# Kernel tuning notes

Hardware: AMD Instinct MI355X
Metric: run time of the kernel (lower is better)

Reference implementation:

```python
import jax, jax.numpy as jnp
import numpy as np

B = 2          # batch size (fixed constant; torch code derives it from coords[:,0].max()+1)
C = 64         # NUM_BEV_FEATURES
NX = NY = 480  # grid_size, nz == 1
NXC = NYC = 960  # hardcoded 'cen' grid


def _make_coords(key, P, b, ny, nx):
    kb, ky, kx = jax.random.split(key, 3)
    bi = jax.random.randint(kb, (P,), 0, b, dtype=jnp.int32)
    z = jnp.zeros((P,), jnp.int32)
    y = jax.random.randint(ky, (P,), 0, ny, dtype=jnp.int32)
    x = jax.random.randint(kx, (P,), 0, nx, dtype=jnp.int32)
    return jnp.stack([bi, z, y, x], axis=1)


def setup_inputs() -> dict:
    key = jax.random.key(0)
    ks = jax.random.split(key, 8)
    return {
        "radar_cen_pillar_features": jax.random.normal(ks[0], (8000, C), jnp.float32),
        "radar_cen_coords": _make_coords(ks[1], 8000, B, NYC, NXC),
        "lidar_cen_pillar_features": jax.random.normal(ks[2], (30000, C), jnp.float32),
        "lidar_cen_coords": _make_coords(ks[3], 30000, B, NYC, NXC),
        "lidar_pillar_features": jax.random.normal(ks[4], (30000, C), jnp.float32),
        "lidar_coords": _make_coords(ks[5], 30000, B, NY, NX),
        "radar_pillar_features": jax.random.normal(ks[6], (8000, C), jnp.float32),
        "radar_coords": _make_coords(ks[7], 8000, B, NY, NX),
    }


def _scatter_bev(feat, coords, ny, nx):
    # feat [P, C], coords [P, 4] = (b, z, y, x); flat index = z + y*nx + x (nz==1 so z==0)
    idx = coords[:, 1] + coords[:, 2] * nx + coords[:, 3]
    grid = jnp.zeros((B, ny * nx, feat.shape[1]), feat.dtype)
    grid = grid.at[coords[:, 0], idx].set(feat)
    # -> [B, C, ny, nx]
    return grid.transpose(0, 2, 1).reshape(B, feat.shape[1], ny, nx)


def _maxpool2(x):
    # AdaptiveMaxPool2d(480) on 960x960 == 2x2 max pool
    b, c, h, w = x.shape
    return x.reshape(b, c, h // 2, 2, w // 2, 2).max(axis=(3, 5))


def reference(radar_cen_pillar_features, radar_cen_coords,
              lidar_cen_pillar_features, lidar_cen_coords,
              lidar_pillar_features, lidar_coords,
              radar_pillar_features, radar_coords):
    radar_cen = _maxpool2(_scatter_bev(radar_cen_pillar_features, radar_cen_coords, NYC, NXC))
    lidar_cen = _maxpool2(_scatter_bev(lidar_cen_pillar_features, lidar_cen_coords, NYC, NXC))
    lidar = _scatter_bev(lidar_pillar_features, lidar_coords, NY, NX)
    radar = _scatter_bev(radar_pillar_features, radar_coords, NY, NX)
    cat = jnp.concatenate(
        [jnp.concatenate([lidar, lidar_cen], axis=1),
         jnp.concatenate([radar, radar_cen], axis=1)], axis=1)
    return lidar, radar, cat
```

## Files before the change

### kernel.cpp

```cpp
#include <hip/hip_runtime.h>

#define NX   480
#define NXC  960
#define NS   (480*480)
#define NSC  (960*960)
#define CC   64
#define BB   2

typedef float f4v __attribute__((ext_vector_type(4)));

__device__ __forceinline__ void nt_store4(float* p, float a, float b, float c, float d) {
    f4v v = {a, b, c, d};
    __builtin_nontemporal_store(v, (f4v*)p);
}

__device__ __forceinline__ f4v ld4(int w, const float* __restrict__ f, int c) {
    f4v z = {0.0f, 0.0f, 0.0f, 0.0f};
    if (w < 0) return z;
    return *(const f4v*)(f + (size_t)w * CC + c);
}

__device__ __forceinline__ f4v max4(f4v a, f4v b) {
    f4v r;
    r.x = fmaxf(a.x, b.x); r.y = fmaxf(a.y, b.y);
    r.z = fmaxf(a.z, b.z); r.w = fmaxf(a.w, b.w);
    return r;
}

struct SrcDesc { const int* coords; int* winner; int P; int nx; int ns; };

__global__ void __launch_bounds__(256)
scatter_winner4(SrcDesc s0, SrcDesc s1, SrcDesc s2, SrcDesc s3) {
    SrcDesc d = (blockIdx.y == 0) ? s0 : (blockIdx.y == 1) ? s1
              : (blockIdx.y == 2) ? s2 : s3;
    int p = blockIdx.x * 256 + threadIdx.x;
    if (p >= d.P) return;
    int b = d.coords[4*p + 0];
    int y = d.coords[4*p + 2];
    int x = d.coords[4*p + 3];
    atomicMax(&d.winner[b*d.ns + y*d.nx + x], p);
}

__global__ void __launch_bounds__(256)
dense_write(const float* __restrict__ lf,  const float* __restrict__ rf,
            const float* __restrict__ lcf, const float* __restrict__ rcf,
            const int* __restrict__ wl,  const int* __restrict__ wr,
            const int* __restrict__ wlc, const int* __restrict__ wrc,
            float* __restrict__ out_l, float* __restrict__ out_r,
            float* __restrict__ out_cat) {
    int s = (blockIdx.x * 256 + threadIdx.x) * 4;
    int b = blockIdx.y;
    int c0 = blockIdx.z * 16;

    int4 v_l = *(const int4*)(wl + (size_t)b*NS + s);
    int4 v_r = *(const int4*)(wr + (size_t)b*NS + s);
    int wla[4] = {v_l.x, v_l.y, v_l.z, v_l.w};
    int wra[4] = {v_r.x, v_r.y, v_r.z, v_r.w};

    int py = s / NX, px = s - py * NX;
    int y0 = py * 2, x0 = px * 2;
    const int* blc = wlc + (size_t)b * NSC;
    const int* brc = wrc + (size_t)b * NSC;
    int4 lt0 = *(const int4*)(blc + (size_t)y0*NXC + x0);
    int4 lt1 = *(const int4*)(blc + (size_t)y0*NXC + x0 + 4);
    int4 lb0 = *(const int4*)(blc + (size_t)(y0+1)*NXC + x0);
    int4 lb1 = *(const int4*)(blc + (size_t)(y0+1)*NXC + x0 + 4);
    int4 rt0 = *(const int4*)(brc + (size_t)y0*NXC + x0);
    int4 rt1 = *(const int4*)(brc + (size_t)y0*NXC + x0 + 4);
    int4 rb0 = *(const int4*)(brc + (size_t)(y0+1)*NXC + x0);
    int4 rb1 = *(const int4*)(brc + (size_t)(y0+1)*NXC + x0 + 4);
    int lct[8] = {lt0.x, lt0.y, lt0.z, lt0.w, lt1.x, lt1.y, lt1.z, lt1.w};
    int lcb[8] = {lb0.x, lb0.y, lb0.z, lb0.w, lb1.x, lb1.y, lb1.z, lb1.w};
    int rct[8] = {rt0.x, rt0.y, rt0.z, rt0.w, rt1.x, rt1.y, rt1.z, rt1.w};
    int rcb[8] = {rb0.x, rb0.y, rb0.z, rb0.w, rb1.x, rb1.y, rb1.z, rb1.w};

    size_t so  = (size_t)b * CC  * NS + s;
    size_t co  = (size_t)b * 256 * NS + s;

    #pragma unroll 1
    for (int g = 0; g < 4; ++g) {
        int c = c0 + g * 4;
        f4v vl[4], vr[4], vlc[4], vrc[4];
        #pragma unroll
        for (int j = 0; j < 4; ++j) {
            vl[j] = ld4(wla[j], lf, c);
            vr[j] = ld4(wra[j], rf, c);
            f4v a = ld4(lct[2*j], lcf, c);
            a = max4(a, ld4(lct[2*j+1], lcf, c));
            a = max4(a, ld4(lcb[2*j],   lcf, c));
            a = max4(a, ld4(lcb[2*j+1], lcf, c));
            vlc[j] = a;
            f4v m = ld4(rct[2*j], rcf, c);
            m = max4(m, ld4(rct[2*j+1], rcf, c));
            m = max4(m, ld4(rcb[2*j],   rcf, c));
            m = max4(m, ld4(rcb[2*j+1], rcf, c));
            vrc[j] = m;
        }
        #pragma unroll
        for (int k = 0; k < 4; ++k) {
            size_t cs = (size_t)(c + k) * NS;
            nt_store4(out_l   + so + cs,                      vl[0][k],  vl[1][k],  vl[2][k],  vl[3][k]);
            nt_store4(out_r   + so + cs,                      vr[0][k],  vr[1][k],  vr[2][k],  vr[3][k]);
            nt_store4(out_cat + co + cs,                      vl[0][k],  vl[1][k],  vl[2][k],  vl[3][k]);
            nt_store4(out_cat + co + (size_t)64*NS  + cs,     vlc[0][k], vlc[1][k], vlc[2][k], vlc[3][k]);
            nt_store4(out_cat + co + (size_t)128*NS + cs,     vr[0][k],  vr[1][k],  vr[2][k],  vr[3][k]);
            nt_store4(out_cat + co + (size_t)192*NS + cs,     vrc[0][k], vrc[1][k], vrc[2][k], vrc[3][k]);
        }
    }
}

extern "C" void kernel_launch(void* const* d_in, const int* in_sizes, int n_in,
                              void* d_out, int out_size, void* d_ws, size_t ws_size,
                              hipStream_t stream) {
    const float* rc_feat   = (const float*)d_in[0];
    const int*   rc_coords = (const int*)  d_in[1];
    const float* lc_feat   = (const float*)d_in[2];
    const int*   lc_coords = (const int*)  d_in[3];
    const float* l_feat    = (const float*)d_in[4];
    const int*   l_coords  = (const int*)  d_in[5];
    const float* r_feat    = (const float*)d_in[6];
    const int*   r_coords  = (const int*)  d_in[7];

    int P_rc = in_sizes[0] / CC;
    int P_lc = in_sizes[2] / CC;
    int P_l  = in_sizes[4] / CC;
    int P_r  = in_sizes[6] / CC;

    float* out_lidar = (float*)d_out;
    float* out_radar = out_lidar + (size_t)BB*CC*NS;
    float* out_cat   = out_radar + (size_t)BB*CC*NS;

    int* w_l  = (int*)d_ws;
    int* w_r  = w_l  + BB*NS;
    int* w_lc = w_r  + BB*NS;
    int* w_rc = w_lc + BB*NSC;
    size_t ws_bytes = (size_t)(2*BB*NS + 2*BB*NSC) * sizeof(int);

    hipMemsetAsync(d_ws, 0xFF, ws_bytes, stream);

    SrcDesc s_l  = { l_coords,  w_l,  P_l,  NX,  NS  };
    SrcDesc s_r  = { r_coords,  w_r,  P_r,  NX,  NS  };
    SrcDesc s_lc = { lc_coords, w_lc, P_lc, NXC, NSC };
    SrcDesc s_rc = { rc_coords, w_rc, P_rc, NXC, NSC };
    int maxP = max(max(P_l, P_r), max(P_lc, P_rc));
    dim3 wgrid((maxP + 255) / 256, 4);
    scatter_winner4<<<wgrid, 256, 0, stream>>>(s_l, s_r, s_lc, s_rc);

    dim3 grid(NS / (256 * 4), BB, 4);
    dense_write<<<grid, 256, 0, stream>>>(l_feat, r_feat, lc_feat, rc_feat,
                                          w_l, w_r, w_lc, w_rc,
                                          out_lidar, out_radar, out_cat);
}
```

Baseline: 730.6 us.

## Replace dense gather-write with memset plus sparse scatter of occupied cells

Instead of a dense pass that reads winner maps for every output cell and writes all channels, the output is zero-filled with hipMemsetAsync and a sparse kernel writes only the cells that hold a winning pillar. The scatter kernel also records a per-pooled-cell winner for the center grids, so each pooled cell is handled once. This drops the dense winner-map reads and the pillar-feature gathers in favour of a memset plus scattered 4-byte stores with a large channel stride. Those stores are poorly coalesced, and the output is still written in full by the memset.

```diff
diff --git a/kernel.cpp b/kernel.cpp
--- a/kernel.cpp
+++ b/kernel.cpp
@@ -9,17 +9,6 @@
 
 typedef float f4v __attribute__((ext_vector_type(4)));
 
-__device__ __forceinline__ void nt_store4(float* p, float a, float b, float c, float d) {
-    f4v v = {a, b, c, d};
-    __builtin_nontemporal_store(v, (f4v*)p);
-}
-
-__device__ __forceinline__ f4v ld4(int w, const float* __restrict__ f, int c) {
-    f4v z = {0.0f, 0.0f, 0.0f, 0.0f};
-    if (w < 0) return z;
-    return *(const f4v*)(f + (size_t)w * CC + c);
-}
-
 __device__ __forceinline__ f4v max4(f4v a, f4v b) {
     f4v r;
     r.x = fmaxf(a.x, b.x); r.y = fmaxf(a.y, b.y);
@@ -27,7 +16,7 @@
     return r;
 }
 
-struct SrcDesc { const int* coords; int* winner; int P; int nx; int ns; };
+struct SrcDesc { const int* coords; int* winner; int* pooled; int P; int nx; int ns; };
 
 __global__ void __launch_bounds__(256)
 scatter_winner4(SrcDesc s0, SrcDesc s1, SrcDesc s2, SrcDesc s3) {
@@ -39,73 +28,71 @@
     int y = d.coords[4*p + 2];
     int x = d.coords[4*p + 3];
     atomicMax(&d.winner[b*d.ns + y*d.nx + x], p);
+    if (d.pooled)
+        atomicMax(&d.pooled[b*NS + (y>>1)*NX + (x>>1)], p);
 }
 
 __global__ void __launch_bounds__(256)
-dense_write(const float* __restrict__ lf,  const float* __restrict__ rf,
-            const float* __restrict__ lcf, const float* __restrict__ rcf,
-            const int* __restrict__ wl,  const int* __restrict__ wr,
-            const int* __restrict__ wlc, const int* __restrict__ wrc,
-            float* __restrict__ out_l, float* __restrict__ out_r,
-            float* __restrict__ out_cat) {
-    int s = (blockIdx.x * 256 + threadIdx.x) * 4;
-    int b = blockIdx.y;
-    int c0 = blockIdx.z * 16;
+sparse_write(const float* __restrict__ lf,  const float* __restrict__ rf,
+             const float* __restrict__ lcf, const float* __restrict__ rcf,
+             const int* __restrict__ l_coords,  const int* __restrict__ r_coords,
+             const int* __restrict__ lc_coords, const int* __restrict__ rc_coords,
+             const int* __restrict__ wl,  const int* __restrict__ wr,
+             const int* __restrict__ wlc, const int* __restrict__ wrc,
+             const int* __restrict__ wplc, const int* __restrict__ wprc,
+             int P_l, int P_r, int P_lc, int P_rc,
+             float* __restrict__ out_l, float* __restrict__ out_r,
+             float* __restrict__ out_cat)
+{
+    int idx = blockIdx.x * 256 + threadIdx.x;
+    int p = idx >> 4;
+    int q = idx & 15;
+    int job = blockIdx.y;
 
-    int4 v_l = *(const int4*)(wl + (size_t)b*NS + s);
-    int4 v_r = *(const int4*)(wr + (size_t)b*NS + s);
-    int wla[4] = {v_l.x, v_l.y, v_l.z, v_l.w};
-    int wra[4] = {v_r.x, v_r.y, v_r.z, v_r.w};
-
-    int py = s / NX, px = s - py * NX;
-    int y0 = py * 2, x0 = px * 2;
-    const int* blc = wlc + (size_t)b * NSC;
-    const int* brc = wrc + (size_t)b * NSC;
-    int4 lt0 = *(const int4*)(blc + (size_t)y0*NXC + x0);
-    int4 lt1 = *(const int4*)(blc + (size_t)y0*NXC + x0 + 4);
-    int4 lb0 = *(const int4*)(blc + (size_t)(y0+1)*NXC + x0);
-    int4 lb1 = *(const int4*)(blc + (size_t)(y0+1)*NXC + x0 + 4);
-    int4 rt0 = *(const int4*)(brc + (size_t)y0*NXC + x0);
-    int4 rt1 = *(const int4*)(brc + (size_t)y0*NXC + x0 + 4);
-    int4 rb0 = *(const int4*)(brc + (size_t)(y0+1)*NXC + x0);
-    int4 rb1 = *(const int4*)(brc + (size_t)(y0+1)*NXC + x0 + 4);
-    int lct[8] = {lt0.x, lt0.y, lt0.z, lt0.w, lt1.x, lt1.y, lt1.z, lt1.w};
-    int lcb[8] = {lb0.x, lb0.y, lb0.z, lb0.w, lb1.x, lb1.y, lb1.z, lb1.w};
-    int rct[8] = {rt0.x, rt0.y, rt0.z, rt0.w, rt1.x, rt1.y, rt1.z, rt1.w};
-    int rcb[8] = {rb0.x, rb0.y, rb0.z, rb0.w, rb1.x, rb1.y, rb1.z, rb1.w};
-
-    size_t so  = (size_t)b * CC  * NS + s;
-    size_t co  = (size_t)b * 256 * NS + s;
-
-    #pragma unroll 1
-    for (int g = 0; g < 4; ++g) {
-        int c = c0 + g * 4;
-        f4v vl[4], vr[4], vlc[4], vrc[4];
-        #pragma unroll
-        for (int j = 0; j < 4; ++j) {
-            vl[j] = ld4(wla[j], lf, c);
-            vr[j] = ld4(wra[j], rf, c);
-            f4v a = ld4(lct[2*j], lcf, c);
-            a = max4(a, ld4(lct[2*j+1], lcf, c));
-            a = max4(a, ld4(lcb[2*j],   lcf, c));
-            a = max4(a, ld4(lcb[2*j+1], lcf, c));
-            vlc[j] = a;
-            f4v m = ld4(rct[2*j], rcf, c);
-            m = max4(m, ld4(rct[2*j+1], rcf, c));
-            m = max4(m, ld4(rcb[2*j],   rcf, c));
-            m = max4(m, ld4(rcb[2*j+1], rcf, c));
-            vrc[j] = m;
-        }
+    if (job < 2) {
+        const float* f      = job ? rf       : lf;
+        const int*   coords = job ? r_coords : l_coords;
+        const int*   w      = job ? wr       : wl;
+        int          P      = job ? P_r      : P_l;
+        if (p >= P) return;
+        int4 c = *(const int4*)(coords + 4*p);
+        int b  = c.x;
+        int sp = c.z * NX + c.w;
+        if (w[b*NS + sp] != p) return;
+        f4v v = *(const f4v*)(f + (size_t)p*CC + 4*q);
+        float* o1 = (job ? out_r : out_l)
+                  + (size_t)b*CC*NS  + (size_t)(4*q)*NS + sp;
+        float* o2 = out_cat
+                  + (size_t)b*256*NS + (size_t)((job ? 128 : 0) + 4*q)*NS + sp;
         #pragma unroll
         for (int k = 0; k < 4; ++k) {
-            size_t cs = (size_t)(c + k) * NS;
-            nt_store4(out_l   + so + cs,                      vl[0][k],  vl[1][k],  vl[2][k],  vl[3][k]);
-            nt_store4(out_r   + so + cs,                      vr[0][k],  vr[1][k],  vr[2][k],  vr[3][k]);
-            nt_store4(out_cat + co + cs,                      vl[0][k],  vl[1][k],  vl[2][k],  vl[3][k]);
-            nt_store4(out_cat + co + (size_t)64*NS  + cs,     vlc[0][k], vlc[1][k], vlc[2][k], vlc[3][k]);
-            nt_store4(out_cat + co + (size_t)128*NS + cs,     vr[0][k],  vr[1][k],  vr[2][k],  vr[3][k]);
-            nt_store4(out_cat + co + (size_t)192*NS + cs,     vrc[0][k], vrc[1][k], vrc[2][k], vrc[3][k]);
+            __builtin_nontemporal_store(v[k], o1 + (size_t)k*NS);
+            __builtin_nontemporal_store(v[k], o2 + (size_t)k*NS);
         }
+    } else {
+        const float* f      = (job == 3) ? rcf       : lcf;
+        const int*   coords = (job == 3) ? rc_coords : lc_coords;
+        const int*   w      = (job == 3) ? wrc       : wlc;
+        const int*   wp     = (job == 3) ? wprc      : wplc;
+        int          P      = (job == 3) ? P_rc      : P_lc;
+        if (p >= P) return;
+        int4 c = *(const int4*)(coords + 4*p);
+        int b  = c.x;
+        int oy = c.z >> 1, ox = c.w >> 1;
+        int o  = oy * NX + ox;
+        if (wp[b*NS + o] != p) return;
+        const int* wg = w + (size_t)b*NSC + (size_t)(oy*2)*NXC + ox*2;
+        int w00 = wg[0], w01 = wg[1], w10 = wg[NXC], w11 = wg[NXC + 1];
+        f4v a = {0.0f, 0.0f, 0.0f, 0.0f};
+        if (w00 >= 0) a = max4(a, *(const f4v*)(f + (size_t)w00*CC + 4*q));
+        if (w01 >= 0) a = max4(a, *(const f4v*)(f + (size_t)w01*CC + 4*q));
+        if (w10 >= 0) a = max4(a, *(const f4v*)(f + (size_t)w10*CC + 4*q));
+        if (w11 >= 0) a = max4(a, *(const f4v*)(f + (size_t)w11*CC + 4*q));
+        float* o2 = out_cat
+                  + (size_t)b*256*NS + (size_t)((job == 3 ? 192 : 64) + 4*q)*NS + o;
+        #pragma unroll
+        for (int k = 0; k < 4; ++k)
+            __builtin_nontemporal_store(a[k], o2 + (size_t)k*NS);
     }
 }
 
@@ -130,24 +117,32 @@
     float* out_radar = out_lidar + (size_t)BB*CC*NS;
     float* out_cat   = out_radar + (size_t)BB*CC*NS;
 
-    int* w_l  = (int*)d_ws;
-    int* w_r  = w_l  + BB*NS;
-    int* w_lc = w_r  + BB*NS;
-    int* w_rc = w_lc + BB*NSC;
-    size_t ws_bytes = (size_t)(2*BB*NS + 2*BB*NSC) * sizeof(int);
+    int* w_l   = (int*)d_ws;
+    int* w_r   = w_l   + (size_t)BB*NS;
+    int* w_plc = w_r   + (size_t)BB*NS;
+    int* w_prc = w_plc + (size_t)BB*NS;
+    int* w_lc  = w_prc + (size_t)BB*NS;
+    int* w_rc  = w_lc  + (size_t)BB*NSC;
+    size_t ws_bytes = ((size_t)4*BB*NS + (size_t)2*BB*NSC) * sizeof(int);
 
     hipMemsetAsync(d_ws, 0xFF, ws_bytes, stream);
 
-    SrcDesc s_l  = { l_coords,  w_l,  P_l,  NX,  NS  };
-    SrcDesc s_r  = { r_coords,  w_r,  P_r,  NX,  NS  };
-    SrcDesc s_lc = { lc_coords, w_lc, P_lc, NXC, NSC };
-    SrcDesc s_rc = { rc_coords, w_rc, P_rc, NXC, NSC };
+    size_t out_bytes = (size_t)BB * NS * (2*CC + 256) * sizeof(float);
+    hipMemsetAsync(d_out, 0, out_bytes, stream);
+
+    SrcDesc s_l  = { l_coords,  w_l,  nullptr, P_l,  NX,  NS  };
+    SrcDesc s_r  = { r_coords,  w_r,  nullptr, P_r,  NX,  NS  };
+    SrcDesc s_lc = { lc_coords, w_lc, w_plc,   P_lc, NXC, NSC };
+    SrcDesc s_rc = { rc_coords, w_rc, w_prc,   P_rc, NXC, NSC };
     int maxP = max(max(P_l, P_r), max(P_lc, P_rc));
     dim3 wgrid((maxP + 255) / 256, 4);
     scatter_winner4<<<wgrid, 256, 0, stream>>>(s_l, s_r, s_lc, s_rc);
 
-    dim3 grid(NS / (256 * 4), BB, 4);
-    dense_write<<<grid, 256, 0, stream>>>(l_feat, r_feat, lc_feat, rc_feat,
-                                          w_l, w_r, w_lc, w_rc,
-                                          out_lidar, out_radar, out_cat);
+    dim3 sgrid((maxP * 16 + 255) / 256, 4);
+    sparse_write<<<sgrid, 256, 0, stream>>>(
+        l_feat, r_feat, lc_feat, rc_feat,
+        l_coords, r_coords, lc_coords, rc_coords,
+        w_l, w_r, w_lc, w_rc, w_plc, w_prc,
+        P_l, P_r, P_lc, P_rc,
+        out_lidar, out_radar, out_cat);
 }
```

Result: slower. 1.017 ms (+39.2%).

## Split dense write into separate direct and pooled-center kernels per source

Applied to the files above, without the earlier changes.

Replaces the single dense kernel, which handled all four sources for a 16-channel slice, with two kernels. One copies the direct lidar/radar features to both outputs and the other max-pools the center grids into the concat tensor, each thread now covering all 64 channels of one source. The aim is lower register pressure and less divergent index loading per thread, and less redundant re-reading of winner indices across channel slices. The cost is an extra kernel launch and fewer blocks per launch, so there is less parallelism to hide memory latency.

```diff
diff --git a/kernel.cpp b/kernel.cpp
--- a/kernel.cpp
+++ b/kernel.cpp
@@ -42,69 +42,80 @@
 }
 
 __global__ void __launch_bounds__(256)
-dense_write(const float* __restrict__ lf,  const float* __restrict__ rf,
-            const float* __restrict__ lcf, const float* __restrict__ rcf,
-            const int* __restrict__ wl,  const int* __restrict__ wr,
-            const int* __restrict__ wlc, const int* __restrict__ wrc,
-            float* __restrict__ out_l, float* __restrict__ out_r,
-            float* __restrict__ out_cat) {
+dense_direct(const float* __restrict__ lf, const float* __restrict__ rf,
+             const int* __restrict__ wl, const int* __restrict__ wr,
+             float* __restrict__ out_l, float* __restrict__ out_r,
+             float* __restrict__ out_cat)
+{
     int s = (blockIdx.x * 256 + threadIdx.x) * 4;
     int b = blockIdx.y;
-    int c0 = blockIdx.z * 16;
+    int z = blockIdx.z;
 
-    int4 v_l = *(const int4*)(wl + (size_t)b*NS + s);
-    int4 v_r = *(const int4*)(wr + (size_t)b*NS + s);
-    int wla[4] = {v_l.x, v_l.y, v_l.z, v_l.w};
-    int wra[4] = {v_r.x, v_r.y, v_r.z, v_r.w};
+    const float* f = z ? rf : lf;
+    const int*   w = z ? wr : wl;
+
+    int4 v = *(const int4*)(w + (size_t)b*NS + s);
+    int wa[4] = {v.x, v.y, v.z, v.w};
+
+    float* o1 = (z ? out_r : out_l) + (size_t)b*CC*NS + s;
+    float* o2 = out_cat + (size_t)b*256*NS + (size_t)(z ? 128 : 0)*NS + s;
+
+    #pragma unroll 2
+    for (int g = 0; g < 16; ++g) {
+        int c = g * 4;
+        f4v x0 = ld4(wa[0], f, c);
+        f4v x1 = ld4(wa[1], f, c);
+        f4v x2 = ld4(wa[2], f, c);
+        f4v x3 = ld4(wa[3], f, c);
+        #pragma unroll
+        for (int k = 0; k < 4; ++k) {
+            size_t cs = (size_t)(c + k) * NS;
+            nt_store4(o1 + cs, x0[k], x1[k], x2[k], x3[k]);
+            nt_store4(o2 + cs, x0[k], x1[k], x2[k], x3[k]);
+        }
+    }
+}
+
+__global__ void __launch_bounds__(256)
+dense_cen(const float* __restrict__ lcf, const float* __restrict__ rcf,
+          const int* __restrict__ wlc, const int* __restrict__ wrc,
+          float* __restrict__ out_cat)
+{
+    int s = (blockIdx.x * 256 + threadIdx.x) * 4;
+    int b = blockIdx.y;
+    int z = blockIdx.z;
+
+    const float* f = z ? rcf : lcf;
+    const int*   w = z ? wrc : wlc;
 
     int py = s / NX, px = s - py * NX;
     int y0 = py * 2, x0 = px * 2;
-    const int* blc = wlc + (size_t)b * NSC;
-    const int* brc = wrc + (size_t)b * NSC;
-    int4 lt0 = *(const int4*)(blc + (size_t)y0*NXC + x0);
-    int4 lt1 = *(const int4*)(blc + (size_t)y0*NXC + x0 + 4);
-    int4 lb0 = *(const int4*)(blc + (size_t)(y0+1)*NXC + x0);
-    int4 lb1 = *(const int4*)(blc + (size_t)(y0+1)*NXC + x0 + 4);
-    int4 rt0 = *(const int4*)(brc + (size_t)y0*NXC + x0);
-    int4 rt1 = *(const int4*)(brc + (size_t)y0*NXC + x0 + 4);
-    int4 rb0 = *(const int4*)(brc + (size_t)(y0+1)*NXC + x0);
-    int4 rb1 = *(const int4*)(brc + (size_t)(y0+1)*NXC + x0 + 4);
-    int lct[8] = {lt0.x, lt0.y, lt0.z, lt0.w, lt1.x, lt1.y, lt1.z, lt1.w};
-    int lcb[8] = {lb0.x, lb0.y, lb0.z, lb0.w, lb1.x, lb1.y, lb1.z, lb1.w};
-    int rct[8] = {rt0.x, rt0.y, rt0.z, rt0.w, rt1.x, rt1.y, rt1.z, rt1.w};
-    int rcb[8] = {rb0.x, rb0.y, rb0.z, rb0.w, rb1.x, rb1.y, rb1.z, rb1.w};
+    const int* wb = w + (size_t)b * NSC;
+    int4 t0 = *(const int4*)(wb + (size_t)y0*NXC + x0);
+    int4 t1 = *(const int4*)(wb + (size_t)y0*NXC + x0 + 4);
+    int4 b0 = *(const int4*)(wb + (size_t)(y0+1)*NXC + x0);
+    int4 b1 = *(const int4*)(wb + (size_t)(y0+1)*NXC + x0 + 4);
+    int wt[8] = {t0.x, t0.y, t0.z, t0.w, t1.x, t1.y, t1.z, t1.w};
+    int wbm[8] = {b0.x, b0.y, b0.z, b0.w, b1.x, b1.y, b1.z, b1.w};
 
-    size_t so  = (size_t)b * CC  * NS + s;
-    size_t co  = (size_t)b * 256 * NS + s;
+    float* o2 = out_cat + (size_t)b*256*NS + (size_t)(z ? 192 : 64)*NS + s;
 
     #pragma unroll 1
-    for (int g = 0; g < 4; ++g) {
-        int c = c0 + g * 4;
-        f4v vl[4], vr[4], vlc[4], vrc[4];
+    for (int g = 0; g < 16; ++g) {
+        int c = g * 4;
+        f4v a[4];
         #pragma unroll
         for (int j = 0; j < 4; ++j) {
-            vl[j] = ld4(wla[j], lf, c);
-            vr[j] = ld4(wra[j], rf, c);
-            f4v a = ld4(lct[2*j], lcf, c);
-            a = max4(a, ld4(lct[2*j+1], lcf, c));
-            a = max4(a, ld4(lcb[2*j],   lcf, c));
-            a = max4(a, ld4(lcb[2*j+1], lcf, c));
-            vlc[j] = a;
-            f4v m = ld4(rct[2*j], rcf, c);
-            m = max4(m, ld4(rct[2*j+1], rcf, c));
-            m = max4(m, ld4(rcb[2*j],   rcf, c));
-            m = max4(m, ld4(rcb[2*j+1], rcf, c));
-            vrc[j] = m;
+            f4v m = ld4(wt[2*j], f, c);
+            m = max4(m, ld4(wt[2*j+1],  f, c));
+            m = max4(m, ld4(wbm[2*j],   f, c));
+            m = max4(m, ld4(wbm[2*j+1], f, c));
+            a[j] = m;
         }
         #pragma unroll
         for (int k = 0; k < 4; ++k) {
             size_t cs = (size_t)(c + k) * NS;
-            nt_store4(out_l   + so + cs,                      vl[0][k],  vl[1][k],  vl[2][k],  vl[3][k]);
-            nt_store4(out_r   + so + cs,                      vr[0][k],  vr[1][k],  vr[2][k],  vr[3][k]);
-            nt_store4(out_cat + co + cs,                      vl[0][k],  vl[1][k],  vl[2][k],  vl[3][k]);
-            nt_store4(out_cat + co + (size_t)64*NS  + cs,     vlc[0][k], vlc[1][k], vlc[2][k], vlc[3][k]);
-            nt_store4(out_cat + co + (size_t)128*NS + cs,     vr[0][k],  vr[1][k],  vr[2][k],  vr[3][k]);
-            nt_store4(out_cat + co + (size_t)192*NS + cs,     vrc[0][k], vrc[1][k], vrc[2][k], vrc[3][k]);
+            nt_store4(o2 + cs, a[0][k], a[1][k], a[2][k], a[3][k]);
         }
     }
 }
@@ -146,8 +157,8 @@
     dim3 wgrid((maxP + 255) / 256, 4);
     scatter_winner4<<<wgrid, 256, 0, stream>>>(s_l, s_r, s_lc, s_rc);
 
-    dim3 grid(NS / (256 * 4), BB, 4);
-    dense_write<<<grid, 256, 0, stream>>>(l_feat, r_feat, lc_feat, rc_feat,
-                                          w_l, w_r, w_lc, w_rc,
-                                          out_lidar, out_radar, out_cat);
+    dim3 grid(NS / (256 * 4), BB, 2);
+    dense_direct<<<grid, 256, 0, stream>>>(l_feat, r_feat, w_l, w_r,
+                                           out_lidar, out_radar, out_cat);
+    dense_cen<<<grid, 256, 0, stream>>>(lc_feat, rc_feat, w_lc, w_rc, out_cat);
 }
```

Result: no change. 741.9 us (+1.6%).
